# Kernel optimization log

Measured on AMD Instinct MI355X. Metric: run time of the kernel, lower is better.

The kernel has to match this reference:

```python
import jax, jax.numpy as jnp
import numpy as np

N = 131072  # B*L nodes
H = 256     # hidden_dim


def setup_inputs() -> dict:
    key = jax.random.key(0)
    ks = jax.random.split(key, 13)
    s = 0.02
    return {
        "h": jax.random.normal(ks[0], (N, H), jnp.float32),
        "pos": jax.random.normal(ks[1], (N, 3), jnp.float32),
        # edge_mlp: Linear(2H+1 -> H), SiLU, Linear(H -> H)
        "ew1": jax.random.normal(ks[2], (2 * H + 1, H), jnp.float32) * s,
        "eb1": jnp.zeros((H,), jnp.float32),
        "ew2": jax.random.normal(ks[3], (H, H), jnp.float32) * s,
        "eb2": jnp.zeros((H,), jnp.float32),
        # pos_mlp: Linear(H -> H), SiLU, Linear(H -> 3, bias=False)
        "pw1": jax.random.normal(ks[4], (H, H), jnp.float32) * s,
        "pb1": jnp.zeros((H,), jnp.float32),
        "pw2": jax.random.normal(ks[5], (H, 3), jnp.float32) * s,
        # node_mlp: Linear(2H -> H), SiLU, Linear(H -> H)
        "nw1": jax.random.normal(ks[6], (2 * H, H), jnp.float32) * s,
        "nb1": jnp.zeros((H,), jnp.float32),
        "nw2": jax.random.normal(ks[7], (H, H), jnp.float32) * s,
        "nb2": jnp.zeros((H,), jnp.float32),
    }


def reference(h, pos, ew1, eb1, ew2, eb2, pw1, pb1, pw2, nw1, nb1, nw2, nb2):
    # Chain edges: row = 0..N-2, col = 1..N-1 -> slices instead of gathers.
    rel_pos = pos[1:] - pos[:-1]                                   # [N-1, 3]
    dist = jnp.linalg.norm(rel_pos, axis=-1, keepdims=True)        # [N-1, 1]
    edge_feat = jnp.concatenate([h[:-1], h[1:], dist], axis=-1)    # [N-1, 2H+1]
    edge_attr = jax.nn.silu(edge_feat @ ew1 + eb1) @ ew2 + eb2     # [N-1, H]
    delta_pos = jax.nn.silu(edge_attr @ pw1 + pb1) @ pw2           # [N-1, 3]

    hd = h.shape[1]
    z3 = jnp.zeros((1, 3), pos.dtype)
    zH = jnp.zeros((1, hd), h.dtype)
    # scatter-add over unique chain indices == padded shifts
    pos_update = jnp.concatenate([delta_pos, z3], 0) - jnp.concatenate([z3, delta_pos], 0)
    node_update = jnp.concatenate([edge_attr, zH], 0) + jnp.concatenate([zH, edge_attr], 0)

    h_cat = jnp.concatenate([h, node_update], axis=-1)             # [N, 2H]
    h_out = jax.nn.silu(h_cat @ nw1 + nb1) @ nw2 + nb2             # [N, H]
    pos_out = pos + 0.1 * pos_update                               # [N, 3]
    return h_out, pos_out
```

## Files before the change

kernel.cpp:

```cpp
#include <hip/hip_runtime.h>
#include <hip/hip_bf16.h>
#include <math.h>

#define NN 131072
#define HD 256

typedef __bf16 bf16;
typedef __attribute__((ext_vector_type(8))) __bf16 bf16x8;
typedef __attribute__((ext_vector_type(4))) __bf16 bf16x4;
typedef __attribute__((ext_vector_type(4))) float f32x4;

__device__ __forceinline__ float silu_f(float x) { return x / (1.f + __expf(-x)); }

__device__ __forceinline__ float bfu2f(unsigned int lo16) {
    unsigned int u = lo16 << 16;
    return __builtin_bit_cast(float, u);
}
__device__ __forceinline__ unsigned short f2bfu(float f) {
    bf16 b = (bf16)f;
    return __builtin_bit_cast(unsigned short, b);
}

template<int KSTEPS, int LDA>
__device__ __forceinline__ void mm_tile(const bf16* Xl, int bk0, const bf16x8* __restrict__ Bp,
                                        int wave, int lane, f32x4 acc[4][4]) {
    const int lrow = lane & 15, lkhi = lane >> 4;
    #pragma unroll
    for (int ks = 0; ks < KSTEPS; ++ks) {
        bf16x8 a[4];
        #pragma unroll
        for (int r = 0; r < 4; ++r)
            a[r] = *(const bf16x8*)&Xl[(r * 16 + lrow) * LDA + ks * 32 + lkhi * 8];
        #pragma unroll
        for (int c = 0; c < 4; ++c) {
            bf16x8 b = Bp[((bk0 + ks) * 16 + wave * 4 + c) * 64 + lane];
            #pragma unroll
            for (int r = 0; r < 4; ++r)
                acc[r][c] = __builtin_amdgcn_mfma_f32_16x16x32_bf16(a[r], b, acc[r][c], 0, 0, 0);
        }
    }
}

__device__ __forceinline__ void packW(const float* __restrict__ W, bf16* __restrict__ P, int idx) {
    int j  = idx & 7;
    int ln = (idx >> 3) & 63;
    int cb = (idx >> 9) & 15;
    int ks = idx >> 13;
    int k = ks * 32 + ((ln >> 4) << 3) + j;
    int n = (cb << 4) + (ln & 15);
    P[idx] = (bf16)W[k * HD + n];
}

__global__ void pack_kernel(const float* __restrict__ ew1, const float* __restrict__ ew2,
                            const float* __restrict__ pw1, const float* __restrict__ nw1,
                            const float* __restrict__ nw2,
                            bf16* __restrict__ ew1p, bf16* __restrict__ ew2p,
                            bf16* __restrict__ pw1p, bf16* __restrict__ nw1p,
                            bf16* __restrict__ nw2p) {
    int t = blockIdx.x * 256 + threadIdx.x;
    if (t < 131072) { packW(ew1, ew1p, t); return; }
    t -= 131072;
    if (t < 65536)  { packW(ew2, ew2p, t); return; }
    t -= 65536;
    if (t < 65536)  { packW(pw1, pw1p, t); return; }
    t -= 65536;
    if (t < 131072) { packW(nw1, nw1p, t); return; }
    t -= 131072;
    if (t < 65536)  { packW(nw2, nw2p, t); return; }
}

__global__ __launch_bounds__(256, 4) void edge_kernel(
    const float* __restrict__ h, const float* __restrict__ pos,
    const float* __restrict__ ew1, const float* __restrict__ eb1,
    const float* __restrict__ eb2, const float* __restrict__ pb1,
    const float* __restrict__ pw2,
    const bf16x8* __restrict__ ew1p, const bf16x8* __restrict__ ew2p,
    const bf16x8* __restrict__ pw1p, const bf16x8* __restrict__ nw1p,
    bf16* __restrict__ q1_g, uint2* __restrict__ p1_g,
    float* __restrict__ dp_g) {
    __shared__ bf16 X[65 * 264];
    __shared__ float dist_s[64];
    __shared__ float dp_s[4][64][3];

    const int tid = threadIdx.x;
    const int lane = tid & 63, wave = tid >> 6;
    const int lrow = lane & 15, lkhi = lane >> 4;
    const int e0 = blockIdx.x * 64;

    for (int idx = tid; idx < 65 * 64; idx += 256) {
        int r = idx >> 6, c4 = (idx & 63) << 2;
        int gr = e0 + r;
        float4 v = make_float4(0.f, 0.f, 0.f, 0.f);
        if (gr < NN) v = *(const float4*)&h[(size_t)gr * HD + c4];
        bf16x4 b;
        b[0] = (bf16)v.x; b[1] = (bf16)v.y; b[2] = (bf16)v.z; b[3] = (bf16)v.w;
        *(bf16x4*)&X[r * 264 + c4] = b;
    }
    if (tid < 64) {
        int e = e0 + tid;
        float d = 0.f;
        if (e < NN - 1) {
            float dx = pos[3 * e + 3] - pos[3 * e];
            float dy = pos[3 * e + 4] - pos[3 * e + 1];
            float dz = pos[3 * e + 5] - pos[3 * e + 2];
            d = sqrtf(dx * dx + dy * dy + dz * dz);
        }
        dist_s[tid] = d;
    }
    __syncthreads();

    f32x4 acc[4][4];

    #pragma unroll
    for (int r = 0; r < 4; ++r)
        #pragma unroll
        for (int c = 0; c < 4; ++c) acc[r][c] = (f32x4)0.f;
    mm_tile<8, 264>(X, 0, nw1p, wave, lane, acc);
    {
        uint2* p1w = p1_g + ((size_t)blockIdx.x * 4 + wave) * 1024;
        #pragma unroll
        for (int r = 0; r < 4; ++r)
            #pragma unroll
            for (int c = 0; c < 4; ++c) {
                uint2 v;
                v.x = (unsigned int)f2bfu(acc[r][c][0]) | ((unsigned int)f2bfu(acc[r][c][1]) << 16);
                v.y = (unsigned int)f2bfu(acc[r][c][2]) | ((unsigned int)f2bfu(acc[r][c][3]) << 16);
                p1w[(r * 4 + c) * 64 + lane] = v;
            }
    }

    #pragma unroll
    for (int r = 0; r < 4; ++r)
        #pragma unroll
        for (int c = 0; c < 4; ++c) acc[r][c] = (f32x4)0.f;
    #pragma unroll
    for (int ks = 0; ks < 16; ++ks) {
        const int rb = (ks >= 8) ? 1 : 0;
        const int kk = ks * 32 + lkhi * 8 - rb * 256;
        bf16x8 a[4];
        #pragma unroll
        for (int r = 0; r < 4; ++r)
            a[r] = *(const bf16x8*)&X[(r * 16 + lrow + rb) * 264 + kk];
        #pragma unroll
        for (int c = 0; c < 4; ++c) {
            bf16x8 b = ew1p[(ks * 16 + wave * 4 + c) * 64 + lane];
            #pragma unroll
            for (int r = 0; r < 4; ++r)
                acc[r][c] = __builtin_amdgcn_mfma_f32_16x16x32_bf16(a[r], b, acc[r][c], 0, 0, 0);
        }
    }
    float bias1[4], wlast[4], w2l[4][3];
    #pragma unroll
    for (int c = 0; c < 4; ++c) {
        int col = (wave * 4 + c) * 16 + lrow;
        bias1[c] = eb1[col];
        wlast[c] = ew1[512 * HD + col];
        #pragma unroll
        for (int x = 0; x < 3; ++x) w2l[c][x] = pw2[col * 3 + x];
    }
    __syncthreads();
    #pragma unroll
    for (int r = 0; r < 4; ++r)
        #pragma unroll
        for (int c = 0; c < 4; ++c)
            #pragma unroll
            for (int q = 0; q < 4; ++q) {
                int row = r * 16 + lkhi * 4 + q;
                int col = (wave * 4 + c) * 16 + lrow;
                float v = acc[r][c][q] + dist_s[row] * wlast[c] + bias1[c];
                X[row * 264 + col] = (bf16)silu_f(v);
            }
    __syncthreads();

    #pragma unroll
    for (int r = 0; r < 4; ++r)
        #pragma unroll
        for (int c = 0; c < 4; ++c) acc[r][c] = (f32x4)0.f;
    mm_tile<8, 264>(X, 0, ew2p, wave, lane, acc);
    float bias2[4];
    #pragma unroll
    for (int c = 0; c < 4; ++c) bias2[c] = eb2[(wave * 4 + c) * 16 + lrow];
    __syncthreads();
    #pragma unroll
    for (int r = 0; r < 4; ++r)
        #pragma unroll
        for (int c = 0; c < 4; ++c)
            #pragma unroll
            for (int q = 0; q < 4; ++q) {
                int row = r * 16 + lkhi * 4 + q;
                int col = (wave * 4 + c) * 16 + lrow;
                X[row * 264 + col] = (bf16)(acc[r][c][q] + bias2[c]);
            }
    __syncthreads();

    #pragma unroll
    for (int r = 0; r < 4; ++r)
        #pragma unroll
        for (int c = 0; c < 4; ++c) acc[r][c] = (f32x4)0.f;
    mm_tile<8, 264>(X, 0, pw1p, wave, lane, acc);
    float bias3[4];
    #pragma unroll
    for (int c = 0; c < 4; ++c) bias3[c] = pb1[(wave * 4 + c) * 16 + lrow];

    #pragma unroll
    for (int r = 0; r < 4; ++r) {
        float red[12];
        #pragma unroll
        for (int q = 0; q < 4; ++q) {
            float t3v[4];
            #pragma unroll
            for (int c = 0; c < 4; ++c) t3v[c] = silu_f(acc[r][c][q] + bias3[c]);
            #pragma unroll
            for (int x = 0; x < 3; ++x) {
                float s = 0.f;
                #pragma unroll
                for (int c = 0; c < 4; ++c) s += t3v[c] * w2l[c][x];
                red[q * 3 + x] = s;
            }
        }
        #pragma unroll
        for (int i = 0; i < 12; ++i) {
            float v = red[i];
            v += __shfl_xor(v, 1);
            v += __shfl_xor(v, 2);
            v += __shfl_xor(v, 4);
            v += __shfl_xor(v, 8);
            red[i] = v;
        }
        if (lrow == 0) {
            #pragma unroll
            for (int q = 0; q < 4; ++q)
                #pragma unroll
                for (int x = 0; x < 3; ++x)
                    dp_s[wave][r * 16 + lkhi * 4 + q][x] = red[q * 3 + x];
        }
    }

    #pragma unroll
    for (int r = 0; r < 4; ++r)
        #pragma unroll
        for (int c = 0; c < 4; ++c) acc[r][c] = (f32x4)0.f;
    mm_tile<8, 264>(X, 8, nw1p, wave, lane, acc);

    __syncthreads();
    #pragma unroll
    for (int r = 0; r < 4; ++r)
        #pragma unroll
        for (int c = 0; c < 4; ++c)
            #pragma unroll
            for (int q = 0; q < 4; ++q) {
                int row = r * 16 + lkhi * 4 + q;
                int col = (wave * 4 + c) * 16 + lrow;
                X[row * 264 + col] = (bf16)acc[r][c][q];
            }
    if (tid < 192) {
        int row = tid / 3, x = tid - row * 3;
        float s = dp_s[0][row][x] + dp_s[1][row][x] + dp_s[2][row][x] + dp_s[3][row][x];
        dp_g[(size_t)(e0 + row) * 3 + x] = s;
    }
    __syncthreads();
    for (int idx = tid; idx < 64 * 128; idx += 256) {
        int r = idx >> 7, cu = idx & 127;
        ((unsigned int*)&q1_g[(size_t)(e0 + r) * HD])[cu] = ((const unsigned int*)&X[r * 264])[cu];
    }
}

__global__ __launch_bounds__(256, 4) void node_kernel(
    const float* __restrict__ pos,
    const float* __restrict__ nb1, const float* __restrict__ nb2,
    const bf16x8* __restrict__ nw2p,
    const bf16* __restrict__ q1_g, const uint2* __restrict__ p1_g,
    const float* __restrict__ dp_g,
    float* __restrict__ h_out, float* __restrict__ pos_out) {
    __shared__ bf16 X[65 * 264];

    const int tid = threadIdx.x;
    const int lane = tid & 63, wave = tid >> 6;
    const int lrow = lane & 15, lkhi = lane >> 4;
    const int n0 = blockIdx.x * 64;

    if (tid < 192) {
        int row = tid & 63, col = tid >> 6;
        int i = n0 + row;
        float dpi = (i < NN - 1) ? dp_g[(size_t)i * 3 + col] : 0.f;
        float dpm = (i > 0) ? dp_g[(size_t)(i - 1) * 3 + col] : 0.f;
        pos_out[(size_t)i * 3 + col] = pos[(size_t)i * 3 + col] + 0.1f * (dpi - dpm);
    }

    for (int idx = tid; idx < 65 * 32; idx += 256) {
        int t = idx >> 5, cu = idx & 31;
        int er = n0 - 1 + t;
        uint4 v = make_uint4(0u, 0u, 0u, 0u);
        if (er >= 0 && er <= NN - 2) v = ((const uint4*)&q1_g[(size_t)er * HD])[cu];
        ((uint4*)&X[t * 264])[cu] = v;
    }
    uint2 p1r[16];
    {
        const uint2* p1p = p1_g + ((size_t)blockIdx.x * 4 + wave) * 1024;
        #pragma unroll
        for (int i = 0; i < 16; ++i) p1r[i] = p1p[i * 64 + lane];
    }
    float b1[4];
    #pragma unroll
    for (int c = 0; c < 4; ++c) b1[c] = nb1[(wave * 4 + c) * 16 + lrow];
    __syncthreads();

    unsigned int t4p[32];
    #pragma unroll
    for (int r = 0; r < 4; ++r)
        #pragma unroll
        for (int c = 0; c < 4; ++c) {
            int i = r * 4 + c;
            int col = (wave * 4 + c) * 16 + lrow;
            #pragma unroll
            for (int qh = 0; qh < 2; ++qh) {
                unsigned int pk = qh == 0 ? p1r[i].x : p1r[i].y;
                unsigned int outp = 0;
                #pragma unroll
                for (int j = 0; j < 2; ++j) {
                    int q = 2 * qh + j;
                    int row = r * 16 + lkhi * 4 + q;
                    float p1v = bfu2f(j == 0 ? (pk & 0xffffu) : (pk >> 16));
                    float z = p1v + (float)X[(row + 1) * 264 + col] + (float)X[row * 264 + col] + b1[c];
                    unsigned short tb = f2bfu(silu_f(z));
                    outp |= (unsigned int)tb << (16 * j);
                }
                t4p[i * 2 + qh] = outp;
            }
        }
    __syncthreads();
    #pragma unroll
    for (int r = 0; r < 4; ++r)
        #pragma unroll
        for (int c = 0; c < 4; ++c) {
            int i = r * 4 + c;
            int col = (wave * 4 + c) * 16 + lrow;
            #pragma unroll
            for (int q = 0; q < 4; ++q) {
                int row = r * 16 + lkhi * 4 + q;
                unsigned int pk = t4p[i * 2 + (q >> 1)];
                unsigned short tb = (unsigned short)((q & 1) ? (pk >> 16) : (pk & 0xffffu));
                X[row * 264 + col] = __builtin_bit_cast(bf16, tb);
            }
        }
    __syncthreads();

    f32x4 acc[4][4];
    #pragma unroll
    for (int r = 0; r < 4; ++r)
        #pragma unroll
        for (int c = 0; c < 4; ++c) acc[r][c] = (f32x4)0.f;
    mm_tile<8, 264>(X, 0, nw2p, wave, lane, acc);
    float b2[4];
    #pragma unroll
    for (int c = 0; c < 4; ++c) b2[c] = nb2[(wave * 4 + c) * 16 + lrow];
    #pragma unroll
    for (int r = 0; r < 4; ++r)
        #pragma unroll
        for (int c = 0; c < 4; ++c)
            #pragma unroll
            for (int q = 0; q < 4; ++q) {
                int row = r * 16 + lkhi * 4 + q;
                int col = (wave * 4 + c) * 16 + lrow;
                h_out[(size_t)(n0 + row) * HD + col] = acc[r][c][q] + b2[c];
            }
}

extern "C" void kernel_launch(void* const* d_in, const int* in_sizes, int n_in,
                              void* d_out, int out_size, void* d_ws, size_t ws_size,
                              hipStream_t stream) {
    const float* h   = (const float*)d_in[0];
    const float* pos = (const float*)d_in[1];
    const float* ew1 = (const float*)d_in[2];
    const float* eb1 = (const float*)d_in[3];
    const float* ew2 = (const float*)d_in[4];
    const float* eb2 = (const float*)d_in[5];
    const float* pw1 = (const float*)d_in[6];
    const float* pb1 = (const float*)d_in[7];
    const float* pw2 = (const float*)d_in[8];
    const float* nw1 = (const float*)d_in[9];
    const float* nb1 = (const float*)d_in[10];
    const float* nw2 = (const float*)d_in[11];
    const float* nb2 = (const float*)d_in[12];

    char* ws = (char*)d_ws;
    bf16*  q1   = (bf16*)ws;
    float* dp   = (float*)(ws + 67108864);
    uint2* p1   = (uint2*)(ws + 68681728);
    char*  wsw = ws + 135790592;
    bf16*  ew1p = (bf16*)(wsw);
    bf16*  ew2p = (bf16*)(wsw + 262144);
    bf16*  pw1p = (bf16*)(wsw + 393216);
    bf16*  nw1p = (bf16*)(wsw + 524288);
    bf16*  nw2p = (bf16*)(wsw + 786432);

    float* out = (float*)d_out;
    float* h_out = out;
    float* pos_out = out + (size_t)NN * HD;

    pack_kernel<<<1792, 256, 0, stream>>>(ew1, ew2, pw1, nw1, nw2,
                                          ew1p, ew2p, pw1p, nw1p, nw2p);
    edge_kernel<<<2048, 256, 0, stream>>>(h, pos, ew1, eb1, eb2, pb1, pw2,
                                          (const bf16x8*)ew1p, (const bf16x8*)ew2p,
                                          (const bf16x8*)pw1p, (const bf16x8*)nw1p,
                                          q1, p1, dp);
    node_kernel<<<2048, 256, 0, stream>>>(pos, nb1, nb2,
                                          (const bf16x8*)nw2p,
                                          q1, (const uint2*)p1, dp, h_out, pos_out);
}
```

Baseline: 267.3 us.

## Split column tiles across eight waves per block and reduce delta_pos with LDS atomics

Both kernels now launch 512-thread blocks, so each of the 8 waves computes a 64x32 output slice (2 column tiles) instead of 64x64. This halves the per-wave accumulator and register footprint, with the aim of more latency hiding and wave-level parallelism. The per-wave delta_pos partials are now combined with shared-memory atomicAdds instead of a 4-way staged buffer, and bias loads are hoisted before the first barrier. In exchange, each A fragment read from LDS feeds fewer MFMAs, which raises LDS traffic per flop. The launch_bounds(512,6) register cap is tight and could cause spilling.

```diff
diff --git a/kernel.cpp b/kernel.cpp
--- a/kernel.cpp
+++ b/kernel.cpp
@@ -21,19 +21,19 @@
     return __builtin_bit_cast(unsigned short, b);
 }
 
-template<int KSTEPS, int LDA>
-__device__ __forceinline__ void mm_tile(const bf16* Xl, int bk0, const bf16x8* __restrict__ Bp,
-                                        int wave, int lane, f32x4 acc[4][4]) {
+template<int KSTEPS>
+__device__ __forceinline__ void mm2(const bf16* Xl, int bk0, const bf16x8* __restrict__ Bp,
+                                    int wave, int lane, f32x4 acc[4][2]) {
     const int lrow = lane & 15, lkhi = lane >> 4;
     #pragma unroll
     for (int ks = 0; ks < KSTEPS; ++ks) {
         bf16x8 a[4];
         #pragma unroll
         for (int r = 0; r < 4; ++r)
-            a[r] = *(const bf16x8*)&Xl[(r * 16 + lrow) * LDA + ks * 32 + lkhi * 8];
-        #pragma unroll
-        for (int c = 0; c < 4; ++c) {
-            bf16x8 b = Bp[((bk0 + ks) * 16 + wave * 4 + c) * 64 + lane];
+            a[r] = *(const bf16x8*)&Xl[(r * 16 + lrow) * 264 + ks * 32 + lkhi * 8];
+        #pragma unroll
+        for (int c = 0; c < 2; ++c) {
+            bf16x8 b = Bp[((bk0 + ks) * 16 + wave * 2 + c) * 64 + lane];
             #pragma unroll
             for (int r = 0; r < 4; ++r)
                 acc[r][c] = __builtin_amdgcn_mfma_f32_16x16x32_bf16(a[r], b, acc[r][c], 0, 0, 0);
@@ -69,7 +69,7 @@
     if (t < 65536)  { packW(nw2, nw2p, t); return; }
 }
 
-__global__ __launch_bounds__(256, 4) void edge_kernel(
+__global__ __launch_bounds__(512, 6) void edge_kernel(
     const float* __restrict__ h, const float* __restrict__ pos,
     const float* __restrict__ ew1, const float* __restrict__ eb1,
     const float* __restrict__ eb2, const float* __restrict__ pb1,
@@ -80,14 +80,14 @@
     float* __restrict__ dp_g) {
     __shared__ bf16 X[65 * 264];
     __shared__ float dist_s[64];
-    __shared__ float dp_s[4][64][3];
+    __shared__ float dp_acc[64][3];
 
     const int tid = threadIdx.x;
     const int lane = tid & 63, wave = tid >> 6;
     const int lrow = lane & 15, lkhi = lane >> 4;
     const int e0 = blockIdx.x * 64;
 
-    for (int idx = tid; idx < 65 * 64; idx += 256) {
+    for (int idx = tid; idx < 65 * 64; idx += 512) {
         int r = idx >> 6, c4 = (idx & 63) << 2;
         int gr = e0 + r;
         float4 v = make_float4(0.f, 0.f, 0.f, 0.f);
@@ -106,33 +106,48 @@
             d = sqrtf(dx * dx + dy * dy + dz * dz);
         }
         dist_s[tid] = d;
-    }
-    __syncthreads();
-
-    f32x4 acc[4][4];
-
-    #pragma unroll
-    for (int r = 0; r < 4; ++r)
-        #pragma unroll
-        for (int c = 0; c < 4; ++c) acc[r][c] = (f32x4)0.f;
-    mm_tile<8, 264>(X, 0, nw1p, wave, lane, acc);
+    } else if (tid >= 512 - 192) {
+        int t = tid - (512 - 192);
+        dp_acc[t >> 2][t & 3 ? (t & 3) - 1 : 0] = 0.f;
+    }
+    if (tid < 192) ((float*)dp_acc)[tid] = 0.f;
+    float bias1[2], bias2[2], bias3[2], wlast[2], w2l[2][3];
+    #pragma unroll
+    for (int c = 0; c < 2; ++c) {
+        int col = (wave * 2 + c) * 16 + lrow;
+        bias1[c] = eb1[col];
+        bias2[c] = eb2[col];
+        bias3[c] = pb1[col];
+        wlast[c] = ew1[512 * HD + col];
+        #pragma unroll
+        for (int x = 0; x < 3; ++x) w2l[c][x] = pw2[col * 3 + x];
+    }
+    __syncthreads();
+
+    f32x4 acc[4][2];
+
+    #pragma unroll
+    for (int r = 0; r < 4; ++r)
+        #pragma unroll
+        for (int c = 0; c < 2; ++c) acc[r][c] = (f32x4)0.f;
+    mm2<8>(X, 0, nw1p, wave, lane, acc);
     {
-        uint2* p1w = p1_g + ((size_t)blockIdx.x * 4 + wave) * 1024;
+        uint2* p1w = p1_g + ((size_t)blockIdx.x * 8 + wave) * 512;
         #pragma unroll
         for (int r = 0; r < 4; ++r)
             #pragma unroll
-            for (int c = 0; c < 4; ++c) {
+            for (int c = 0; c < 2; ++c) {
                 uint2 v;
                 v.x = (unsigned int)f2bfu(acc[r][c][0]) | ((unsigned int)f2bfu(acc[r][c][1]) << 16);
                 v.y = (unsigned int)f2bfu(acc[r][c][2]) | ((unsigned int)f2bfu(acc[r][c][3]) << 16);
-                p1w[(r * 4 + c) * 64 + lane] = v;
-            }
-    }
-
-    #pragma unroll
-    for (int r = 0; r < 4; ++r)
-        #pragma unroll
-        for (int c = 0; c < 4; ++c) acc[r][c] = (f32x4)0.f;
+                p1w[(r * 2 + c) * 64 + lane] = v;
+            }
+    }
+
+    #pragma unroll
+    for (int r = 0; r < 4; ++r)
+        #pragma unroll
+        for (int c = 0; c < 2; ++c) acc[r][c] = (f32x4)0.f;
     #pragma unroll
     for (int ks = 0; ks < 16; ++ks) {
         const int rb = (ks >= 8) ? 1 : 0;
@@ -142,31 +157,22 @@
         for (int r = 0; r < 4; ++r)
             a[r] = *(const bf16x8*)&X[(r * 16 + lrow + rb) * 264 + kk];
         #pragma unroll
-        for (int c = 0; c < 4; ++c) {
-            bf16x8 b = ew1p[(ks * 16 + wave * 4 + c) * 64 + lane];
+        for (int c = 0; c < 2; ++c) {
+            bf16x8 b = ew1p[(ks * 16 + wave * 2 + c) * 64 + lane];
             #pragma unroll
             for (int r = 0; r < 4; ++r)
                 acc[r][c] = __builtin_amdgcn_mfma_f32_16x16x32_bf16(a[r], b, acc[r][c], 0, 0, 0);
         }
     }
-    float bias1[4], wlast[4], w2l[4][3];
-    #pragma unroll
-    for (int c = 0; c < 4; ++c) {
-        int col = (wave * 4 + c) * 16 + lrow;
-        bias1[c] = eb1[col];
-        wlast[c] = ew1[512 * HD + col];
-        #pragma unroll
-        for (int x = 0; x < 3; ++x) w2l[c][x] = pw2[col * 3 + x];
-    }
-    __syncthreads();
-    #pragma unroll
-    for (int r = 0; r < 4; ++r)
-        #pragma unroll
-        for (int c = 0; c < 4; ++c)
+    __syncthreads();
+    #pragma unroll
+    for (int r = 0; r < 4; ++r)
+        #pragma unroll
+        for (int c = 0; c < 2; ++c)
             #pragma unroll
             for (int q = 0; q < 4; ++q) {
                 int row = r * 16 + lkhi * 4 + q;
-                int col = (wave * 4 + c) * 16 + lrow;
+                int col = (wave * 2 + c) * 16 + lrow;
                 float v = acc[r][c][q] + dist_s[row] * wlast[c] + bias1[c];
                 X[row * 264 + col] = (bf16)silu_f(v);
             }
@@ -175,20 +181,17 @@
     #pragma unroll
     for (int r = 0; r < 4; ++r)
         #pragma unroll
-        for (int c = 0; c < 4; ++c) acc[r][c] = (f32x4)0.f;
-    mm_tile<8, 264>(X, 0, ew2p, wave, lane, acc);
-    float bias2[4];
-    #pragma unroll
-    for (int c = 0; c < 4; ++c) bias2[c] = eb2[(wave * 4 + c) * 16 + lrow];
-    __syncthreads();
-    #pragma unroll
-    for (int r = 0; r < 4; ++r)
-        #pragma unroll
-        for (int c = 0; c < 4; ++c)
+        for (int c = 0; c < 2; ++c) acc[r][c] = (f32x4)0.f;
+    mm2<8>(X, 0, ew2p, wave, lane, acc);
+    __syncthreads();
+    #pragma unroll
+    for (int r = 0; r < 4; ++r)
+        #pragma unroll
+        for (int c = 0; c < 2; ++c)
             #pragma unroll
             for (int q = 0; q < 4; ++q) {
                 int row = r * 16 + lkhi * 4 + q;
-                int col = (wave * 4 + c) * 16 + lrow;
+                int col = (wave * 2 + c) * 16 + lrow;
                 X[row * 264 + col] = (bf16)(acc[r][c][q] + bias2[c]);
             }
     __syncthreads();
@@ -196,27 +199,19 @@
     #pragma unroll
     for (int r = 0; r < 4; ++r)
         #pragma unroll
-        for (int c = 0; c < 4; ++c) acc[r][c] = (f32x4)0.f;
-    mm_tile<8, 264>(X, 0, pw1p, wave, lane, acc);
-    float bias3[4];
-    #pragma unroll
-    for (int c = 0; c < 4; ++c) bias3[c] = pb1[(wave * 4 + c) * 16 + lrow];
-
+        for (int c = 0; c < 2; ++c) acc[r][c] = (f32x4)0.f;
+    mm2<8>(X, 0, pw1p, wave, lane, acc);
     #pragma unroll
     for (int r = 0; r < 4; ++r) {
         float red[12];
         #pragma unroll
         for (int q = 0; q < 4; ++q) {
-            float t3v[4];
-            #pragma unroll
-            for (int c = 0; c < 4; ++c) t3v[c] = silu_f(acc[r][c][q] + bias3[c]);
-            #pragma unroll
-            for (int x = 0; x < 3; ++x) {
-                float s = 0.f;
-                #pragma unroll
-                for (int c = 0; c < 4; ++c) s += t3v[c] * w2l[c][x];
-                red[q * 3 + x] = s;
-            }
+            float t3v[2];
+            #pragma unroll
+            for (int c = 0; c < 2; ++c) t3v[c] = silu_f(acc[r][c][q] + bias3[c]);
+            #pragma unroll
+            for (int x = 0; x < 3; ++x)
+                red[q * 3 + x] = t3v[0] * w2l[0][x] + t3v[1] * w2l[1][x];
         }
         #pragma unroll
         for (int i = 0; i < 12; ++i) {
@@ -232,40 +227,39 @@
             for (int q = 0; q < 4; ++q)
                 #pragma unroll
                 for (int x = 0; x < 3; ++x)
-                    dp_s[wave][r * 16 + lkhi * 4 + q][x] = red[q * 3 + x];
-        }
-    }
-
-    #pragma unroll
-    for (int r = 0; r < 4; ++r)
-        #pragma unroll
-        for (int c = 0; c < 4; ++c) acc[r][c] = (f32x4)0.f;
-    mm_tile<8, 264>(X, 8, nw1p, wave, lane, acc);
-
-    __syncthreads();
-    #pragma unroll
-    for (int r = 0; r < 4; ++r)
-        #pragma unroll
-        for (int c = 0; c < 4; ++c)
+                    atomicAdd(&dp_acc[r * 16 + lkhi * 4 + q][x], red[q * 3 + x]);
+        }
+    }
+
+    #pragma unroll
+    for (int r = 0; r < 4; ++r)
+        #pragma unroll
+        for (int c = 0; c < 2; ++c) acc[r][c] = (f32x4)0.f;
+    mm2<8>(X, 8, nw1p, wave, lane, acc);
+
+    __syncthreads();
+    #pragma unroll
+    for (int r = 0; r < 4; ++r)
+        #pragma unroll
+        for (int c = 0; c < 2; ++c)
             #pragma unroll
             for (int q = 0; q < 4; ++q) {
                 int row = r * 16 + lkhi * 4 + q;
-                int col = (wave * 4 + c) * 16 + lrow;
+                int col = (wave * 2 + c) * 16 + lrow;
                 X[row * 264 + col] = (bf16)acc[r][c][q];
             }
     if (tid < 192) {
         int row = tid / 3, x = tid - row * 3;
-        float s = dp_s[0][row][x] + dp_s[1][row][x] + dp_s[2][row][x] + dp_s[3][row][x];
-        dp_g[(size_t)(e0 + row) * 3 + x] = s;
-    }
-    __syncthreads();
-    for (int idx = tid; idx < 64 * 128; idx += 256) {
+        dp_g[(size_t)(e0 + row) * 3 + x] = dp_acc[row][x];
+    }
+    __syncthreads();
+    for (int idx = tid; idx < 64 * 128; idx += 512) {
         int r = idx >> 7, cu = idx & 127;
         ((unsigned int*)&q1_g[(size_t)(e0 + r) * HD])[cu] = ((const unsigned int*)&X[r * 264])[cu];
     }
 }
 
-__global__ __launch_bounds__(256, 4) void node_kernel(
+__global__ __launch_bounds__(512, 6) void node_kernel(
     const float* __restrict__ pos,
     const float* __restrict__ nb1, const float* __restrict__ nb2,
     const bf16x8* __restrict__ nw2p,
@@ -287,31 +281,31 @@
         pos_out[(size_t)i * 3 + col] = pos[(size_t)i * 3 + col] + 0.1f * (dpi - dpm);
     }
 
-    for (int idx = tid; idx < 65 * 32; idx += 256) {
+    for (int idx = tid; idx < 65 * 32; idx += 512) {
         int t = idx >> 5, cu = idx & 31;
         int er = n0 - 1 + t;
         uint4 v = make_uint4(0u, 0u, 0u, 0u);
         if (er >= 0 && er <= NN - 2) v = ((const uint4*)&q1_g[(size_t)er * HD])[cu];
         ((uint4*)&X[t * 264])[cu] = v;
     }
-    uint2 p1r[16];
+    uint2 p1r[8];
     {
-        const uint2* p1p = p1_g + ((size_t)blockIdx.x * 4 + wave) * 1024;
-        #pragma unroll
-        for (int i = 0; i < 16; ++i) p1r[i] = p1p[i * 64 + lane];
-    }
-    float b1[4];
-    #pragma unroll
-    for (int c = 0; c < 4; ++c) b1[c] = nb1[(wave * 4 + c) * 16 + lrow];
-    __syncthreads();
-
-    unsigned int t4p[32];
-    #pragma unroll
-    for (int r = 0; r < 4; ++r)
-        #pragma unroll
-        for (int c = 0; c < 4; ++c) {
-            int i = r * 4 + c;
-            int col = (wave * 4 + c) * 16 + lrow;
+        const uint2* p1p = p1_g + ((size_t)blockIdx.x * 8 + wave) * 512;
+        #pragma unroll
+        for (int i = 0; i < 8; ++i) p1r[i] = p1p[i * 64 + lane];
+    }
+    float b1[2];
+    #pragma unroll
+    for (int c = 0; c < 2; ++c) b1[c] = nb1[(wave * 2 + c) * 16 + lrow];
+    __syncthreads();
+
+    unsigned int t4p[16];
+    #pragma unroll
+    for (int r = 0; r < 4; ++r)
+        #pragma unroll
+        for (int c = 0; c < 2; ++c) {
+            int i = r * 2 + c;
+            int col = (wave * 2 + c) * 16 + lrow;
             #pragma unroll
             for (int qh = 0; qh < 2; ++qh) {
                 unsigned int pk = qh == 0 ? p1r[i].x : p1r[i].y;
@@ -332,9 +326,9 @@
     #pragma unroll
     for (int r = 0; r < 4; ++r)
         #pragma unroll
-        for (int c = 0; c < 4; ++c) {
-            int i = r * 4 + c;
-            int col = (wave * 4 + c) * 16 + lrow;
+        for (int c = 0; c < 2; ++c) {
+            int i = r * 2 + c;
+            int col = (wave * 2 + c) * 16 + lrow;
             #pragma unroll
             for (int q = 0; q < 4; ++q) {
                 int row = r * 16 + lkhi * 4 + q;
@@ -345,23 +339,23 @@
         }
     __syncthreads();
 
-    f32x4 acc[4][4];
-    #pragma unroll
-    for (int r = 0; r < 4; ++r)
-        #pragma unroll
-        for (int c = 0; c < 4; ++c) acc[r][c] = (f32x4)0.f;
-    mm_tile<8, 264>(X, 0, nw2p, wave, lane, acc);
-    float b2[4];
-    #pragma unroll
-    for (int c = 0; c < 4; ++c) b2[c] = nb2[(wave * 4 + c) * 16 + lrow];
-    #pragma unroll
-    for (int r = 0; r < 4; ++r)
-        #pragma unroll
-        for (int c = 0; c < 4; ++c)
+    f32x4 acc[4][2];
+    #pragma unroll
+    for (int r = 0; r < 4; ++r)
+        #pragma unroll
+        for (int c = 0; c < 2; ++c) acc[r][c] = (f32x4)0.f;
+    mm2<8>(X, 0, nw2p, wave, lane, acc);
+    float b2[2];
+    #pragma unroll
+    for (int c = 0; c < 2; ++c) b2[c] = nb2[(wave * 2 + c) * 16 + lrow];
+    #pragma unroll
+    for (int r = 0; r < 4; ++r)
+        #pragma unroll
+        for (int c = 0; c < 2; ++c)
             #pragma unroll
             for (int q = 0; q < 4; ++q) {
                 int row = r * 16 + lkhi * 4 + q;
-                int col = (wave * 4 + c) * 16 + lrow;
+                int col = (wave * 2 + c) * 16 + lrow;
                 h_out[(size_t)(n0 + row) * HD + col] = acc[r][c][q] + b2[c];
             }
 }
@@ -400,11 +394,11 @@
 
     pack_kernel<<<1792, 256, 0, stream>>>(ew1, ew2, pw1, nw1, nw2,
                                           ew1p, ew2p, pw1p, nw1p, nw2p);
-    edge_kernel<<<2048, 256, 0, stream>>>(h, pos, ew1, eb1, eb2, pb1, pw2,
+    edge_kernel<<<2048, 512, 0, stream>>>(h, pos, ew1, eb1, eb2, pb1, pw2,
                                           (const bf16x8*)ew1p, (const bf16x8*)ew2p,
                                           (const bf16x8*)pw1p, (const bf16x8*)nw1p,
                                           q1, p1, dp);
-    node_kernel<<<2048, 256, 0, stream>>>(pos, nb1, nb2,
+    node_kernel<<<2048, 512, 0, stream>>>(pos, nb1, nb2,
                                           (const bf16x8*)nw2p,
                                           q1, (const uint2*)p1, dp, h_out, pos_out);
 }
```

After: 488.7 us. +82.9%, slower.
